# Kernel tuning notes

Measured on AMD Instinct MI355X. Metric: run time of the kernel, lower is better.

Reference implementation:

```python
import jax, jax.numpy as jnp
import numpy as np

EPS = 1e-5  # torch InstanceNorm3d default eps


def setup_inputs() -> dict:
    key = jax.random.key(0)
    ks = jax.random.split(key, 7)
    B, C, H, W, D = 2, 128, 48, 48, 48
    c_m, c_n = 128, 64
    return {
        "x": jax.random.normal(ks[0], (B, C, H, W, D), dtype=jnp.float32),
        "WA": jax.random.normal(ks[1], (c_m, C), dtype=jnp.float32) * (1.0 / np.sqrt(C)),
        "bA": jax.random.normal(ks[2], (c_m,), dtype=jnp.float32) * 0.01,
        "WB": jax.random.normal(ks[3], (c_n, C), dtype=jnp.float32) * (1.0 / np.sqrt(C)),
        "bB": jax.random.normal(ks[4], (c_n,), dtype=jnp.float32) * 0.01,
        "WV": jax.random.normal(ks[5], (c_n, C), dtype=jnp.float32) * (1.0 / np.sqrt(C)),
        "bV": jax.random.normal(ks[6], (c_n,), dtype=jnp.float32) * 0.01,
    }


def reference(x, WA, bA, WB, bB, WV, bV):
    B, C, H, W, D = x.shape
    L = H * W * D
    xf = x.reshape(B, C, L)
    # 1x1x1 Conv3d projections == per-voxel linear over channels
    A = jnp.einsum('bcl,mc->bml', xf, WA) + bA[None, :, None]   # (B, c_m, L)
    Bm = jnp.einsum('bcl,nc->bnl', xf, WB) + bB[None, :, None]  # (B, c_n, L)
    V = jnp.einsum('bcl,nc->bnl', xf, WV) + bV[None, :, None]   # (B, c_n, L)
    # attention maps: softmax over spatial positions
    attn_maps = jax.nn.softmax(Bm, axis=-1)                     # (B, c_n, L)
    # global descriptors: A @ attn_maps^T
    G = jnp.einsum('bml,bnl->bmn', A, attn_maps)                # (B, c_m, c_n)
    # attention vectors: softmax over c_n (channel) dim
    attn_vec = jax.nn.softmax(V, axis=1)                        # (B, c_n, L)
    Z = jnp.einsum('bmn,bnl->bml', G, attn_vec)                 # (B, c_m, L)
    # InstanceNorm3d (affine=False, biased variance) per (batch, channel)
    mean = jnp.mean(Z, axis=-1, keepdims=True)
    var = jnp.var(Z, axis=-1, keepdims=True)
    Zn = (Z - mean) * jax.lax.rsqrt(var + EPS)
    return Zn.reshape(B, Z.shape[1], H, W, D)
```

## Files before the change

### kernel.cpp

```cpp
#include <hip/hip_runtime.h>

#define LTOT 110592
#define EPSV 1e-5f

typedef _Float16 f16;
typedef __attribute__((ext_vector_type(4))) _Float16 f16x4;
typedef __attribute__((ext_vector_type(8))) _Float16 f16x8;
typedef __attribute__((ext_vector_type(4))) float f32x4;

#define MFMA16(a, b, c) __builtin_amdgcn_mfma_f32_16x16x32_f16(a, b, c, 0, 0, 0)
#define SWC(c) ((((c) ^ ((c) >> 3)) & 7) << 3)

__device__ __forceinline__ f16x8 ld_w8(const float* p) {
  const float4 a = *(const float4*)p;
  const float4 b = *(const float4*)(p + 4);
  f16x8 f;
  f[0] = (f16)a.x; f[1] = (f16)a.y; f[2] = (f16)a.z; f[3] = (f16)a.w;
  f[4] = (f16)b.x; f[5] = (f16)b.y; f[6] = (f16)b.z; f[7] = (f16)b.w;
  return f;
}

__global__ __launch_bounds__(256, 2) void p1_proj_m(
    const float* __restrict__ x,
    const float* __restrict__ WB_, const float* __restrict__ bB_,
    const float* __restrict__ WV_, const float* __restrict__ bV_,
    f16* __restrict__ av_g, float* __restrict__ mpart, float* __restrict__ separt)
{
  __shared__ __align__(16) f16 XT[64 * 128 + 2240];
  __shared__ __align__(16) f16 XC[128 * 64];
  __shared__ __align__(16) f16 EL[64 * 64];
  __shared__ __align__(16) f16 AVT[64 * 64];
  __shared__ float colp[4][64];
  const int tid = threadIdx.x, b = blockIdx.y, blk = blockIdx.x;
  const int ln = tid & 63, w = tid >> 6, g = ln >> 4;

  const int nB = w * 16 + (ln & 15);
  f16x8 wbf[4], wvf[4];
  #pragma unroll
  for (int ks = 0; ks < 4; ++ks) {
    wbf[ks] = ld_w8(&WB_[nB * 128 + ks * 32 + g * 8]);
    wvf[ks] = ld_w8(&WV_[nB * 128 + ks * 32 + g * 8]);
  }
  const float sB = bB_[nB];
  float biasV[4];
  #pragma unroll
  for (int r = 0; r < 4; ++r) biasV[r] = bV_[w * 16 + g * 4 + r];

  f32x4 macc[8];
  #pragma unroll
  for (int i = 0; i < 8; ++i) macc[i] = (f32x4){0.f, 0.f, 0.f, 0.f};
  float se = 0.f;

  const int co = tid >> 4, LQ = tid & 15;
  const size_t xb = (size_t)b * 128 * LTOT;

  float4 xr[8];
  {
    const int l0 = blk * 256;
    #pragma unroll
    for (int j = 0; j < 8; ++j)
      xr[j] = *(const float4*)&x[xb + (size_t)(co * 8 + j) * LTOT + l0 + LQ * 4];
  }

  for (int t = 0; t < 4; ++t) {
    const int l0 = (blk * 4 + t) * 64;
    __syncthreads();
    #pragma unroll
    for (int i = 0; i < 4; ++i) {
      const int l = LQ * 4 + i;
      f16x8 v;
      #pragma unroll
      for (int j = 0; j < 8; ++j) v[j] = (f16)(((const float*)&xr[j])[i]);
      *(f16x8*)&XT[l * 128 + ((co * 8) ^ ((l & 7) << 3))] = v;
    }
    #pragma unroll
    for (int j = 0; j < 8; ++j) {
      const int c = co * 8 + j;
      f16x4 q;
      q[0] = (f16)xr[j].x; q[1] = (f16)xr[j].y;
      q[2] = (f16)xr[j].z; q[3] = (f16)xr[j].w;
      *(f16x4*)&XC[c * 64 + ((LQ * 4) ^ SWC(c))] = q;
    }
    __syncthreads();
    if (t < 3) {
      const int l0n = l0 + 64;
      #pragma unroll
      for (int j = 0; j < 8; ++j)
        xr[j] = *(const float4*)&x[xb + (size_t)(co * 8 + j) * LTOT + l0n + LQ * 4];
    }
    f32x4 aB[4], aV[4];
    #pragma unroll
    for (int lt = 0; lt < 4; ++lt) {
      aB[lt] = (f32x4){0.f, 0.f, 0.f, 0.f};
      aV[lt] = (f32x4){0.f, 0.f, 0.f, 0.f};
      const int l = lt * 16 + (ln & 15);
      #pragma unroll
      for (int ks = 0; ks < 4; ++ks) {
        const f16x8 xf = *(const f16x8*)&XT[l * 128 + (((ks * 4 + g) * 8) ^ ((l & 7) << 3))];
        aB[lt] = MFMA16(xf, wbf[ks], aB[lt]);
        aV[lt] = MFMA16(wvf[ks], xf, aV[lt]);
      }
    }
    #pragma unroll
    for (int lt = 0; lt < 4; ++lt) {
      f16x4 ev4;
      #pragma unroll
      for (int r = 0; r < 4; ++r) {
        const float e = __expf(aB[lt][r] + sB);
        se += e;
        ev4[r] = (f16)e;
      }
      const int lq = lt * 16 + g * 4;
      *(f16x4*)&EL[nB * 64 + (lq ^ ((nB & 7) << 3))] = ev4;
    }
    float cs[4];
    #pragma unroll
    for (int ct = 0; ct < 4; ++ct) {
      f16x4 av4;
      float s = 0.f;
      #pragma unroll
      for (int r = 0; r < 4; ++r) {
        const float e = __expf(aV[ct][r] + biasV[r]);
        s += e;
        av4[r] = (f16)e;
      }
      cs[ct] = s;
      const int l = ct * 16 + (ln & 15);
      *(f16x4*)&AVT[l * 64 + ((w * 16 + g * 4) ^ ((l & 7) << 3))] = av4;
    }
    #pragma unroll
    for (int ct = 0; ct < 4; ++ct) {
      cs[ct] += __shfl_xor(cs[ct], 16);
      cs[ct] += __shfl_xor(cs[ct], 32);
    }
    {
      const float v = (g == 0) ? cs[0] : (g == 1) ? cs[1] : (g == 2) ? cs[2] : cs[3];
      colp[w][g * 16 + (ln & 15)] = v;
    }
    __syncthreads();
    {
      const int l = tid >> 2, q = tid & 3;
      const float rs = 1.f / (colp[0][l] + colp[1][l] + colp[2][l] + colp[3][l]);
      f16x8 a0 = *(const f16x8*)&AVT[l * 64 + ((q * 16) ^ ((l & 7) << 3))];
      f16x8 a1 = *(const f16x8*)&AVT[l * 64 + ((q * 16 + 8) ^ ((l & 7) << 3))];
      #pragma unroll
      for (int j = 0; j < 8; ++j) {
        a0[j] = (f16)((float)a0[j] * rs);
        a1[j] = (f16)((float)a1[j] * rs);
      }
      f16* gp = av_g + ((size_t)b * LTOT + l0 + l) * 64 + q * 16;
      *(f16x8*)&gp[0] = a0;
      *(f16x8*)&gp[8] = a1;
    }
    {
      f16x8 el[2];
      #pragma unroll
      for (int ks = 0; ks < 2; ++ks)
        el[ks] = *(const f16x8*)&EL[nB * 64 + ((ks * 32 + g * 8) ^ ((nB & 7) << 3))];
      #pragma unroll
      for (int cblk = 0; cblk < 8; ++cblk) {
        const int c = cblk * 16 + (ln & 15);
        #pragma unroll
        for (int ks = 0; ks < 2; ++ks) {
          const f16x8 xcf = *(const f16x8*)&XC[c * 64 + ((ks * 32 + g * 8) ^ SWC(c))];
          macc[cblk] = MFMA16(el[ks], xcf, macc[cblk]);
        }
      }
    }
  }
  float* mp = mpart + (size_t)(b * 432 + blk) * 8192;
  #pragma unroll
  for (int cblk = 0; cblk < 8; ++cblk)
    #pragma unroll
    for (int r = 0; r < 4; ++r)
      mp[(w * 16 + g * 4 + r) * 128 + cblk * 16 + (ln & 15)] = macc[cblk][r];
  se += __shfl_xor(se, 16);
  se += __shfl_xor(se, 32);
  if (ln < 16) separt[(size_t)(b * 432 + blk) * 64 + w * 16 + ln] = se;
}

__global__ void p2a(const float* __restrict__ mpart, const float* __restrict__ separt,
                    float* __restrict__ mpart2, float* __restrict__ sesum)
{
  const int b = blockIdx.y, bx = blockIdx.x, tid = threadIdx.x;
  if (bx < 256) {
    const int seg = bx >> 5, chunk = bx & 31;
    const int idx = chunk * 256 + tid;
    float s = 0.f;
    for (int j = 0; j < 54; ++j)
      s += mpart[(size_t)(b * 432 + seg * 54 + j) * 8192 + idx];
    mpart2[(size_t)(b * 8 + seg) * 8192 + idx] = s;
  } else if (tid < 64) {
    float s = 0.f;
    for (int k = 0; k < 432; ++k) s += separt[(size_t)(b * 432 + k) * 64 + tid];
    sesum[b * 64 + tid] = s;
  }
}

__global__ void p2a2(const float* __restrict__ mpart2, float* __restrict__ msum)
{
  const int b = blockIdx.y;
  const int idx = blockIdx.x * 256 + threadIdx.x;
  float s = 0.f;
  #pragma unroll
  for (int k = 0; k < 8; ++k) s += mpart2[(size_t)(b * 8 + k) * 8192 + idx];
  msum[(size_t)b * 8192 + idx] = s;
}

__global__ void p2b(const float* __restrict__ WA_, const float* __restrict__ bA_,
                    const float* __restrict__ msum, const float* __restrict__ sesum,
                    float* __restrict__ g32, f16* __restrict__ g16)
{
  const int b = blockIdx.y;
  const int idx = blockIdx.x * 256 + threadIdx.x;
  const int m = idx >> 6, n = idx & 63;
  float s = 0.f;
  #pragma unroll 4
  for (int c = 0; c < 128; ++c) s += WA_[m * 128 + c] * msum[(size_t)b * 8192 + n * 128 + c];
  const float gv = s / sesum[b * 64 + n] + bA_[m];
  g32[(size_t)b * 8192 + m * 64 + n] = gv;
  g16[(size_t)b * 8192 + m * 64 + (n ^ ((m & 7) << 3))] = (f16)gv;
}

__global__ __launch_bounds__(256, 2) void p3_cov(
    const f16* __restrict__ av_g, float* __restrict__ cpart, float* __restrict__ mupart)
{
  __shared__ __align__(16) f16 AV[64 * 64];
  const int tid = threadIdx.x, b = blockIdx.y, blk = blockIdx.x;
  const int ln = tid & 63, w = tid >> 6, g = ln >> 4;
  const int nq4 = (tid & 15) * 4, lq4 = (tid >> 4) * 4;
  const int nmu = tid >> 2, qmu = tid & 3;

  f32x4 cacc[4];
  #pragma unroll
  for (int j = 0; j < 4; ++j) cacc[j] = (f32x4){0.f, 0.f, 0.f, 0.f};
  float muacc = 0.f;

  for (int t = 0; t < 8; ++t) {
    const int l0 = (blk * 8 + t) * 64;
    __syncthreads();
    {
      f16x4 rd[4];
      #pragma unroll
      for (int i = 0; i < 4; ++i)
        rd[i] = *(const f16x4*)&av_g[((size_t)b * LTOT + l0 + lq4 + i) * 64 + nq4];
      #pragma unroll
      for (int j = 0; j < 4; ++j) {
        const int n = nq4 + j;
        f16x4 wr;
        #pragma unroll
        for (int i = 0; i < 4; ++i) wr[i] = rd[i][j];
        *(f16x4*)&AV[n * 64 + (lq4 ^ ((n & 7) << 3))] = wr;
      }
    }
    __syncthreads();
    {
      const f16x8 a0 = *(const f16x8*)&AV[nmu * 64 + ((qmu * 16) ^ ((nmu & 7) << 3))];
      const f16x8 a1 = *(const f16x8*)&AV[nmu * 64 + ((qmu * 16 + 8) ^ ((nmu & 7) << 3))];
      #pragma unroll
      for (int j = 0; j < 8; ++j) muacc += (float)a0[j] + (float)a1[j];
    }
    const int nA = w * 16 + (ln & 15);
    f16x8 caf[2];
    #pragma unroll
    for (int ks = 0; ks < 2; ++ks)
      caf[ks] = *(const f16x8*)&AV[nA * 64 + ((ks * 32 + g * 8) ^ ((nA & 7) << 3))];
    #pragma unroll
    for (int nct = 0; nct < 4; ++nct) {
      const int nb = nct * 16 + (ln & 15);
      #pragma unroll
      for (int ks = 0; ks < 2; ++ks) {
        const f16x8 cbf = *(const f16x8*)&AV[nb * 64 + ((ks * 32 + g * 8) ^ ((nb & 7) << 3))];
        cacc[nct] = MFMA16(caf[ks], cbf, cacc[nct]);
      }
    }
  }
  float* cp = cpart + (size_t)(b * 216 + blk) * 4096;
  #pragma unroll
  for (int nct = 0; nct < 4; ++nct)
    #pragma unroll
    for (int r = 0; r < 4; ++r)
      cp[(w * 16 + g * 4 + r) * 64 + nct * 16 + (ln & 15)] = cacc[nct][r];
  muacc += __shfl_xor(muacc, 1);
  muacc += __shfl_xor(muacc, 2);
  if (qmu == 0) mupart[(size_t)(b * 216 + blk) * 64 + nmu] = muacc;
}

__global__ void p4a(const float* __restrict__ cpart, const float* __restrict__ mupart,
                    float* __restrict__ csum, float* __restrict__ musum)
{
  const int b = blockIdx.y, bx = blockIdx.x, tid = threadIdx.x;
  if (bx < 64) {
    const int idx = bx * 64 + (tid >> 2), q = tid & 3;
    float s = 0.f;
    for (int k = q; k < 216; k += 4) s += cpart[(size_t)(b * 216 + k) * 4096 + idx];
    s += __shfl_xor(s, 1);
    s += __shfl_xor(s, 2);
    if (q == 0) csum[(size_t)b * 4096 + idx] = s;
  } else if (tid < 64) {
    float s = 0.f;
    for (int k = 0; k < 216; ++k) s += mupart[(size_t)(b * 216 + k) * 64 + tid];
    musum[b * 64 + tid] = s;
  }
}

__global__ void p4b(const float* __restrict__ csum, const float* __restrict__ musum,
                    const float* __restrict__ g32, float* __restrict__ mr)
{
  __shared__ __align__(16) float CL[4096];
  __shared__ __align__(16) float GLs[32 * 68];
  __shared__ float MUL[64];
  const int tid = threadIdx.x, b = blockIdx.y, bx = blockIdx.x;
  #pragma unroll
  for (int k = 0; k < 16; ++k) CL[k * 256 + tid] = csum[(size_t)b * 4096 + k * 256 + tid];
  #pragma unroll
  for (int k = 0; k < 8; ++k) {
    const int idx = k * 256 + tid;
    const int m_ = idx >> 6, n_ = idx & 63;
    GLs[m_ * 68 + n_] = g32[(size_t)b * 8192 + (bx * 32 + m_) * 64 + n_];
  }
  if (tid < 64) MUL[tid] = musum[b * 64 + tid];
  __syncthreads();
  const int mrow = (tid >> 3) * 68, oct = tid & 7;
  float q = 0.f;
  #pragma unroll
  for (int q4 = 0; q4 < 2; ++q4) {
    const int npb = oct * 8 + q4 * 4;
    float t0 = 0.f, t1 = 0.f, t2 = 0.f, t3 = 0.f;
    #pragma unroll 8
    for (int n = 0; n < 64; ++n) {
      const float4 cv = *(const float4*)&CL[n * 64 + npb];
      const float gv = GLs[mrow + n];
      t0 += gv * cv.x; t1 += gv * cv.y; t2 += gv * cv.z; t3 += gv * cv.w;
    }
    const float4 gq = *(const float4*)&GLs[mrow + npb];
    q += t0 * gq.x + t1 * gq.y + t2 * gq.z + t3 * gq.w;
  }
  q += __shfl_xor(q, 1); q += __shfl_xor(q, 2); q += __shfl_xor(q, 4);
  if (oct == 0) {
    float meanq = 0.f;
    #pragma unroll 8
    for (int n = 0; n < 64; ++n) meanq += GLs[mrow + n] * MUL[n];
    const int m = bx * 32 + (tid >> 3);
    const float mean = meanq / (float)LTOT;
    const float var = fmaxf(q / (float)LTOT - mean * mean, 0.f);
    mr[(b * 128 + m) * 2] = mean;
    mr[(b * 128 + m) * 2 + 1] = rsqrtf(var + EPSV);
  }
}

__global__ __launch_bounds__(256, 2) void p5_z(
    const f16* __restrict__ av_g, const f16* __restrict__ g16,
    const float* __restrict__ mr, float* __restrict__ out)
{
  __shared__ __align__(16) f16 AVT[64 * 64];
  const int tid = threadIdx.x, b = blockIdx.y, blk = blockIdx.x;
  const int ln = tid & 63, w = tid >> 6, g = ln >> 4;
  const int lst = tid & 63, pst = tid >> 6;

  f16x8 gf[2][2];
  float mean_[2][4], rsig_[2][4];
  #pragma unroll
  for (int mct = 0; mct < 2; ++mct) {
    const int mA = w * 32 + mct * 16 + (ln & 15);
    #pragma unroll
    for (int ks = 0; ks < 2; ++ks)
      gf[mct][ks] = *(const f16x8*)&g16[(size_t)b * 8192 + mA * 64 +
                                        (((ks * 4 + g) * 8) ^ ((mA & 7) << 3))];
    #pragma unroll
    for (int r = 0; r < 4; ++r) {
      const int m = w * 32 + mct * 16 + g * 4 + r;
      mean_[mct][r] = mr[(b * 128 + m) * 2];
      rsig_[mct][r] = mr[(b * 128 + m) * 2 + 1];
    }
  }

  for (int t = 0; t < 4; ++t) {
    const int l0 = (blk * 4 + t) * 64;
    __syncthreads();
    {
      const f16* gp = av_g + ((size_t)b * LTOT + l0 + lst) * 64 + pst * 16;
      const f16x8 a0 = *(const f16x8*)&gp[0];
      const f16x8 a1 = *(const f16x8*)&gp[8];
      *(f16x8*)&AVT[lst * 64 + ((pst * 16) ^ ((lst & 7) << 3))] = a0;
      *(f16x8*)&AVT[lst * 64 + ((pst * 16 + 8) ^ ((lst & 7) << 3))] = a1;
    }
    __syncthreads();
    #pragma unroll
    for (int lt = 0; lt < 4; ++lt) {
      const int l = lt * 16 + (ln & 15);
      f16x8 avf[2];
      #pragma unroll
      for (int ks = 0; ks < 2; ++ks)
        avf[ks] = *(const f16x8*)&AVT[l * 64 + (((ks * 4 + g) * 8) ^ ((l & 7) << 3))];
      #pragma unroll
      for (int mct = 0; mct < 2; ++mct) {
        f32x4 z = {0.f, 0.f, 0.f, 0.f};
        #pragma unroll
        for (int ks = 0; ks < 2; ++ks) z = MFMA16(gf[mct][ks], avf[ks], z);
        #pragma unroll
        for (int r = 0; r < 4; ++r) {
          const int m = w * 32 + mct * 16 + g * 4 + r;
          out[(size_t)(b * 128 + m) * LTOT + l0 + l] =
              (z[r] - mean_[mct][r]) * rsig_[mct][r];
        }
      }
    }
  }
}

extern "C" void kernel_launch(void* const* d_in, const int* in_sizes, int n_in,
                              void* d_out, int out_size, void* d_ws, size_t ws_size,
                              hipStream_t stream)
{
  const float* x  = (const float*)d_in[0];
  const float* WA = (const float*)d_in[1];
  const float* bA = (const float*)d_in[2];
  const float* WB = (const float*)d_in[3];
  const float* bB = (const float*)d_in[4];
  const float* WV = (const float*)d_in[5];
  const float* bV = (const float*)d_in[6];
  float* out = (float*)d_out;

  float* w = (float*)d_ws;
  float* mpart  = w;
  float* mpart2 = mpart + 7077888;
  float* separt = mpart2 + 131072;
  float* msum   = separt + 55296;
  float* sesum  = msum + 16384;
  float* g32    = sesum + 128;
  f16*   g16f   = (f16*)(g32 + 16384);
  f16*   av_g   = g16f + 16384;
  float* cpart  = (float*)(av_g + 14155776);
  float* mupart = cpart + 1769472;
  float* csum   = mupart + 27648;
  float* musum  = csum + 8192;
  float* mr     = musum + 128;

  p1_proj_m<<<dim3(432, 2), 256, 0, stream>>>(x, WB, bB, WV, bV, av_g, mpart, separt);
  p2a<<<dim3(257, 2), 256, 0, stream>>>(mpart, separt, mpart2, sesum);
  p2a2<<<dim3(32, 2), 256, 0, stream>>>(mpart2, msum);
  p2b<<<dim3(32, 2), 256, 0, stream>>>(WA, bA, msum, sesum, g32, g16f);
  p3_cov<<<dim3(216, 2), 256, 0, stream>>>(av_g, cpart, mupart);
  p4a<<<dim3(65, 2), 256, 0, stream>>>(cpart, mupart, csum, musum);
  p4b<<<dim3(4, 2), 256, 0, stream>>>(csum, musum, g32, mr);
  p5_z<<<dim3(432, 2), 256, 0, stream>>>(av_g, g16f, mr, out);
}
```

Before: 123.7 us.

## Merge independent reduction and covariance kernels into shared launches

```diff
diff --git a/kernel.cpp b/kernel.cpp
--- a/kernel.cpp
+++ b/kernel.cpp
@@ -179,54 +179,31 @@
   if (ln < 16) separt[(size_t)(b * 432 + blk) * 64 + w * 16 + ln] = se;
 }
 
-__global__ void p2a(const float* __restrict__ mpart, const float* __restrict__ separt,
-                    float* __restrict__ mpart2, float* __restrict__ sesum)
-{
-  const int b = blockIdx.y, bx = blockIdx.x, tid = threadIdx.x;
-  if (bx < 256) {
-    const int seg = bx >> 5, chunk = bx & 31;
-    const int idx = chunk * 256 + tid;
-    float s = 0.f;
-    for (int j = 0; j < 54; ++j)
-      s += mpart[(size_t)(b * 432 + seg * 54 + j) * 8192 + idx];
-    mpart2[(size_t)(b * 8 + seg) * 8192 + idx] = s;
-  } else if (tid < 64) {
-    float s = 0.f;
-    for (int k = 0; k < 432; ++k) s += separt[(size_t)(b * 432 + k) * 64 + tid];
-    sesum[b * 64 + tid] = s;
-  }
-}
-
-__global__ void p2a2(const float* __restrict__ mpart2, float* __restrict__ msum)
-{
-  const int b = blockIdx.y;
-  const int idx = blockIdx.x * 256 + threadIdx.x;
-  float s = 0.f;
-  #pragma unroll
-  for (int k = 0; k < 8; ++k) s += mpart2[(size_t)(b * 8 + k) * 8192 + idx];
-  msum[(size_t)b * 8192 + idx] = s;
-}
-
-__global__ void p2b(const float* __restrict__ WA_, const float* __restrict__ bA_,
-                    const float* __restrict__ msum, const float* __restrict__ sesum,
-                    float* __restrict__ g32, f16* __restrict__ g16)
-{
-  const int b = blockIdx.y;
-  const int idx = blockIdx.x * 256 + threadIdx.x;
-  const int m = idx >> 6, n = idx & 63;
-  float s = 0.f;
-  #pragma unroll 4
-  for (int c = 0; c < 128; ++c) s += WA_[m * 128 + c] * msum[(size_t)b * 8192 + n * 128 + c];
-  const float gv = s / sesum[b * 64 + n] + bA_[m];
-  g32[(size_t)b * 8192 + m * 64 + n] = gv;
-  g16[(size_t)b * 8192 + m * 64 + (n ^ ((m & 7) << 3))] = (f16)gv;
-}
-
-__global__ __launch_bounds__(256, 2) void p3_cov(
-    const f16* __restrict__ av_g, float* __restrict__ cpart, float* __restrict__ mupart)
+__global__ __launch_bounds__(256, 2) void ka_red_cov(
+    const float* __restrict__ mpart, const float* __restrict__ separt,
+    float* __restrict__ mpart2, float* __restrict__ sesum,
+    const f16* __restrict__ av_g, float* __restrict__ cpart,
+    float* __restrict__ mupart)
 {
   __shared__ __align__(16) f16 AV[64 * 64];
-  const int tid = threadIdx.x, b = blockIdx.y, blk = blockIdx.x;
+  const int bxa = blockIdx.x, b = blockIdx.y, tid = threadIdx.x;
+  if (bxa < 257) {
+    const int bx = bxa;
+    if (bx < 256) {
+      const int seg = bx >> 5, chunk = bx & 31;
+      const int idx = chunk * 256 + tid;
+      float s = 0.f;
+      for (int j = 0; j < 54; ++j)
+        s += mpart[(size_t)(b * 432 + seg * 54 + j) * 8192 + idx];
+      mpart2[(size_t)(b * 8 + seg) * 8192 + idx] = s;
+    } else if (tid < 64) {
+      float s = 0.f;
+      for (int k = 0; k < 432; ++k) s += separt[(size_t)(b * 432 + k) * 64 + tid];
+      sesum[b * 64 + tid] = s;
+    }
+    return;
+  }
+  const int blk = bxa - 257;
   const int ln = tid & 63, w = tid >> 6, g = ln >> 4;
   const int nq4 = (tid & 15) * 4, lq4 = (tid >> 4) * 4;
   const int nmu = tid >> 2, qmu = tid & 3;
@@ -286,10 +263,20 @@
   if (qmu == 0) mupart[(size_t)(b * 216 + blk) * 64 + nmu] = muacc;
 }
 
-__global__ void p4a(const float* __restrict__ cpart, const float* __restrict__ mupart,
-                    float* __restrict__ csum, float* __restrict__ musum)
-{
-  const int b = blockIdx.y, bx = blockIdx.x, tid = threadIdx.x;
+__global__ void kb_red(const float* __restrict__ mpart2, float* __restrict__ msum,
+                       const float* __restrict__ cpart, const float* __restrict__ mupart,
+                       float* __restrict__ csum, float* __restrict__ musum)
+{
+  const int bxa = blockIdx.x, b = blockIdx.y, tid = threadIdx.x;
+  if (bxa < 32) {
+    const int idx = bxa * 256 + tid;
+    float s = 0.f;
+    #pragma unroll
+    for (int k = 0; k < 8; ++k) s += mpart2[(size_t)(b * 8 + k) * 8192 + idx];
+    msum[(size_t)b * 8192 + idx] = s;
+    return;
+  }
+  const int bx = bxa - 32;
   if (bx < 64) {
     const int idx = bx * 64 + (tid >> 2), q = tid & 3;
     float s = 0.f;
@@ -302,6 +289,21 @@
     for (int k = 0; k < 216; ++k) s += mupart[(size_t)(b * 216 + k) * 64 + tid];
     musum[b * 64 + tid] = s;
   }
+}
+
+__global__ void p2b(const float* __restrict__ WA_, const float* __restrict__ bA_,
+                    const float* __restrict__ msum, const float* __restrict__ sesum,
+                    float* __restrict__ g32, f16* __restrict__ g16)
+{
+  const int b = blockIdx.y;
+  const int idx = blockIdx.x * 256 + threadIdx.x;
+  const int m = idx >> 6, n = idx & 63;
+  float s = 0.f;
+  #pragma unroll 4
+  for (int c = 0; c < 128; ++c) s += WA_[m * 128 + c] * msum[(size_t)b * 8192 + n * 128 + c];
+  const float gv = s / sesum[b * 64 + n] + bA_[m];
+  g32[(size_t)b * 8192 + m * 64 + n] = gv;
+  g16[(size_t)b * 8192 + m * 64 + (n ^ ((m & 7) << 3))] = (f16)gv;
 }
 
 __global__ void p4b(const float* __restrict__ csum, const float* __restrict__ musum,
@@ -438,11 +440,10 @@
   float* mr     = musum + 128;
 
   p1_proj_m<<<dim3(432, 2), 256, 0, stream>>>(x, WB, bB, WV, bV, av_g, mpart, separt);
-  p2a<<<dim3(257, 2), 256, 0, stream>>>(mpart, separt, mpart2, sesum);
-  p2a2<<<dim3(32, 2), 256, 0, stream>>>(mpart2, msum);
+  ka_red_cov<<<dim3(473, 2), 256, 0, stream>>>(mpart, separt, mpart2, sesum,
+                                               av_g, cpart, mupart);
+  kb_red<<<dim3(97, 2), 256, 0, stream>>>(mpart2, msum, cpart, mupart, csum, musum);
   p2b<<<dim3(32, 2), 256, 0, stream>>>(WA, bA, msum, sesum, g32, g16f);
-  p3_cov<<<dim3(216, 2), 256, 0, stream>>>(av_g, cpart, mupart);
-  p4a<<<dim3(65, 2), 256, 0, stream>>>(cpart, mupart, csum, musum);
   p4b<<<dim3(4, 2), 256, 0, stream>>>(csum, musum, g32, mr);
   p5_z<<<dim3(432, 2), 256, 0, stream>>>(av_g, g16f, mr, out);
 }
```

Measured after the change: 113.1 us. 1.09x faster.
